# Performance work log

Measured on AMD Instinct MI355X. Metric: run time of the kernel, lower is better.

The kernel has to match this reference:

```python
import jax, jax.numpy as jnp
import numpy as np

THRESHOLD = 0.05

def binarize101(w, threshold):
    # Ternary quantization to {-1, 0, +1}: zero inside the dead-zone [-thr, thr].
    pos = (w > threshold).astype(w.dtype)
    neg = (w < -threshold).astype(w.dtype)
    return pos - neg

def setup_inputs() -> dict:
    key = jax.random.key(0)
    k1, k2, k3 = jax.random.split(key, 3)
    x = jax.random.normal(k1, (8192, 4096), dtype=jnp.float32)
    weight = jax.random.normal(k2, (4096, 4096), dtype=jnp.float32)
    bias = jax.random.normal(k3, (4096,), dtype=jnp.float32)
    return {"x": x, "weight": weight, "bias": bias}

def reference(x, weight, bias):
    wb = binarize101(weight, THRESHOLD)
    # F.linear: x @ wb.T + bias ; x: [N, in], weight: [out, in] -> [N, out]
    return jnp.einsum('ni,oi->no', x, wb) + bias
```

## Files before the change

kernel.cpp:

```cpp
#include <hip/hip_runtime.h>

typedef float floatx4 __attribute__((ext_vector_type(4)));
typedef __bf16 bf16x8 __attribute__((ext_vector_type(8)));
using u16 = unsigned short;
using u32 = unsigned int;

#define GLOBAL_AS __attribute__((address_space(1)))
#define LDS_AS    __attribute__((address_space(3)))

__global__ void cvt_x_kernel(const float* __restrict__ x, u16* __restrict__ xb, int n8) {
  int stride = gridDim.x * blockDim.x;
  for (int i = blockIdx.x * blockDim.x + threadIdx.x; i < n8; i += stride) {
    const float4* p = (const float4*)(x + (size_t)i * 8);
    float4 a = p[0], b = p[1];
    float v[8] = {a.x, a.y, a.z, a.w, b.x, b.y, b.z, b.w};
    u32 r[8];
#pragma unroll
    for (int j = 0; j < 8; ++j) {
      u32 u = __float_as_uint(v[j]);
      r[j] = (u + 0x7FFFu + ((u >> 16) & 1u)) >> 16;
    }
    uint4 o;
    o.x = r[0] | (r[1] << 16);
    o.y = r[2] | (r[3] << 16);
    o.z = r[4] | (r[5] << 16);
    o.w = r[6] | (r[7] << 16);
    *(uint4*)(xb + (size_t)i * 8) = o;
  }
}

__global__ void quant_w_kernel(const float* __restrict__ w, u16* __restrict__ wb, int n8) {
  int stride = gridDim.x * blockDim.x;
  for (int i = blockIdx.x * blockDim.x + threadIdx.x; i < n8; i += stride) {
    const float4* p = (const float4*)(w + (size_t)i * 8);
    float4 a = p[0], b = p[1];
    float v[8] = {a.x, a.y, a.z, a.w, b.x, b.y, b.z, b.w};
    u32 r[8];
#pragma unroll
    for (int j = 0; j < 8; ++j) {
      r[j] = (v[j] > 0.05f) ? 0x3F80u : ((v[j] < -0.05f) ? 0xBF80u : 0u);
    }
    uint4 o;
    o.x = r[0] | (r[1] << 16);
    o.y = r[2] | (r[3] << 16);
    o.z = r[4] | (r[5] << 16);
    o.w = r[6] | (r[7] << 16);
    *(uint4*)(wb + (size_t)i * 8) = o;
  }
}

__global__ __launch_bounds__(512, 2) void gemm_bin_8ph(
    const u16* __restrict__ A, const u16* __restrict__ B,
    const float* __restrict__ bias, float* __restrict__ C,
    int M, int N, int K) {
  __shared__ u16 lds[65536];

  const int tid = threadIdx.x;
  const int w = tid >> 6, l = tid & 63;
  const int wr = w >> 2, wc = w & 3;
  const int r = l & 15;

  const int nbn = N >> 8;
  int wg = blockIdx.x;
  const int nwg = gridDim.x;
  if ((nwg & 7) == 0) wg = (wg & 7) * (nwg >> 3) + (wg >> 3);
  const int bm = wg / nbn, bn = wg % nbn;

  const int NSTEPS = K >> 5;

  const int prow = ((tid >> 6) << 4) + (tid & 15);
  const int pk = ((tid >> 4) & 3) << 3;
  const size_t Abase = (size_t)(bm * 256 + prow) * K + pk;
  const size_t Bbase = (size_t)(bn * 256 + prow) * K + pk;
  const size_t chunkStride = (size_t)128 * K;

  const u16* const ldsA = lds + wr * 4096 + l * 8;
  const u16* const ldsB = lds + 8192 + wc * 2048 + l * 8;

  floatx4 acc[8][4] = {};

  for (int u = 0; u < 4; ++u) {
    const int so = u * 16384;
    const u16* ga = A + Abase + (size_t)u * 32;
    const u16* gb = B + Bbase + (size_t)u * 32;
    __builtin_amdgcn_global_load_lds((const GLOBAL_AS void*)ga,
                                     (LDS_AS void*)(lds + so + tid * 8), 16, 0, 0);
    __builtin_amdgcn_global_load_lds((const GLOBAL_AS void*)(ga + chunkStride),
                                     (LDS_AS void*)(lds + so + 4096 + tid * 8), 16, 0, 0);
    __builtin_amdgcn_global_load_lds((const GLOBAL_AS void*)gb,
                                     (LDS_AS void*)(lds + so + 8192 + tid * 8), 16, 0, 0);
    __builtin_amdgcn_global_load_lds((const GLOBAL_AS void*)(gb + chunkStride),
                                     (LDS_AS void*)(lds + so + 12288 + tid * 8), 16, 0, 0);
  }
  asm volatile("s_waitcnt vmcnt(12)" ::: "memory");
  __builtin_amdgcn_s_barrier();

  for (int s = 0; s < NSTEPS; ++s) {
    const int so = (s & 3) * 16384;
    const bool doSt = (s >= 1) && (s + 3 < NSTEPS);
    const int son = ((s + 3) & 3) * 16384;
    const u16* gaN = A + Abase + (size_t)(s + 3) * 32;
    const u16* gbN = B + Bbase + (size_t)(s + 3) * 32;

    bf16x8 af[8], bf[4];
#pragma unroll
    for (int m = 0; m < 4; ++m) af[m] = *(const bf16x8*)(ldsA + so + m * 512);
#pragma unroll
    for (int n = 0; n < 4; ++n) bf[n] = *(const bf16x8*)(ldsB + so + n * 512);
    if (doSt) {
      __builtin_amdgcn_global_load_lds((const GLOBAL_AS void*)gaN,
                                       (LDS_AS void*)(lds + son + tid * 8), 16, 0, 0);
      __builtin_amdgcn_global_load_lds((const GLOBAL_AS void*)(gaN + chunkStride),
                                       (LDS_AS void*)(lds + son + 4096 + tid * 8), 16, 0, 0);
    }
    __builtin_amdgcn_s_barrier();
    asm volatile("s_waitcnt lgkmcnt(0)" ::: "memory");
    __builtin_amdgcn_sched_barrier(0);
    __builtin_amdgcn_s_setprio(1);
#pragma unroll
    for (int m = 0; m < 4; ++m)
#pragma unroll
      for (int n = 0; n < 4; ++n)
        acc[m][n] = __builtin_amdgcn_mfma_f32_16x16x32_bf16(af[m], bf[n], acc[m][n], 0, 0, 0);
    __builtin_amdgcn_s_setprio(0);
    __builtin_amdgcn_s_barrier();

#pragma unroll
    for (int m = 4; m < 8; ++m) af[m] = *(const bf16x8*)(ldsA + so + m * 512);
    if (doSt) {
      __builtin_amdgcn_global_load_lds((const GLOBAL_AS void*)gbN,
                                       (LDS_AS void*)(lds + son + 8192 + tid * 8), 16, 0, 0);
      __builtin_amdgcn_global_load_lds((const GLOBAL_AS void*)(gbN + chunkStride),
                                       (LDS_AS void*)(lds + son + 12288 + tid * 8), 16, 0, 0);
    }
    __builtin_amdgcn_s_barrier();
    asm volatile("s_waitcnt lgkmcnt(0)" ::: "memory");
    __builtin_amdgcn_sched_barrier(0);
    __builtin_amdgcn_s_setprio(1);
#pragma unroll
    for (int m = 4; m < 8; ++m)
#pragma unroll
      for (int n = 0; n < 4; ++n)
        acc[m][n] = __builtin_amdgcn_mfma_f32_16x16x32_bf16(af[m], bf[n], acc[m][n], 0, 0, 0);
    __builtin_amdgcn_s_setprio(0);
    if (s + 1 < NSTEPS) {
      if (s + 3 < NSTEPS)      asm volatile("s_waitcnt vmcnt(8)" ::: "memory");
      else if (s + 2 < NSTEPS) asm volatile("s_waitcnt vmcnt(4)" ::: "memory");
      else                     asm volatile("s_waitcnt vmcnt(0)" ::: "memory");
      __builtin_amdgcn_s_barrier();
    }
  }

  const int g = l >> 4;
  const int colb = bn * 256 + wc * 64;
  float bv[4];
#pragma unroll
  for (int n = 0; n < 4; ++n) bv[n] = bias[colb + n * 16 + r];
  const int rowb0 = bm * 256 + wr * 128;
#pragma unroll
  for (int m = 0; m < 8; ++m) {
    const int rowb = rowb0 + m * 16 + g * 4;
#pragma unroll
    for (int n = 0; n < 4; ++n) {
      const int col = colb + n * 16 + r;
      float* cp = C + (size_t)rowb * N + col;
#pragma unroll
      for (int q = 0; q < 4; ++q) cp[(size_t)q * N] = acc[m][n][q] + bv[n];
    }
  }
}

__global__ void gemm_naive_kernel(const float* __restrict__ x, const float* __restrict__ wgt,
                                  const float* __restrict__ bias, float* __restrict__ out,
                                  int M, int N, int K) {
  long long idx = (long long)blockIdx.x * blockDim.x + threadIdx.x;
  if (idx >= (long long)M * N) return;
  int o = (int)(idx % N);
  int m = (int)(idx / N);
  const float* xr = x + (size_t)m * K;
  const float* wr = wgt + (size_t)o * K;
  float s = 0.f;
  for (int i = 0; i < K; ++i) {
    float wv = wr[i];
    float t = (wv > 0.05f) ? 1.f : ((wv < -0.05f) ? -1.f : 0.f);
    s = fmaf(xr[i], t, s);
  }
  out[idx] = s + bias[o];
}

extern "C" void kernel_launch(void* const* d_in, const int* in_sizes, int n_in,
                              void* d_out, int out_size, void* d_ws, size_t ws_size,
                              hipStream_t stream) {
  const float* x    = (const float*)d_in[0];
  const float* wgt  = (const float*)d_in[1];
  const float* bias = (const float*)d_in[2];
  float* out = (float*)d_out;

  const int N = in_sizes[2];
  const int K = in_sizes[1] / N;
  const int M = in_sizes[0] / K;

  const size_t need = ((size_t)M * K + (size_t)N * K) * sizeof(u16);
  if (ws_size >= need && (M % 256 == 0) && (N % 256 == 0) && (K % 32 == 0) && K >= 128) {
    u16* xb = (u16*)d_ws;
    u16* wb = xb + (size_t)M * K;
    const int nx8 = (M * K) / 8;
    const int nw8 = (N * K) / 8;
    cvt_x_kernel<<<2048, 256, 0, stream>>>(x, xb, nx8);
    quant_w_kernel<<<2048, 256, 0, stream>>>(wgt, wb, nw8);
    const int grid = (M / 256) * (N / 256);
    gemm_bin_8ph<<<grid, 512, 0, stream>>>(xb, wb, bias, out, M, N, K);
  } else {
    const long long total = (long long)M * N;
    gemm_naive_kernel<<<(unsigned)((total + 255) / 256), 256, 0, stream>>>(x, wgt, bias, out, M, N, K);
  }
}
```

Before: 314.0 us.

## Double-buffer LDS fragments in registers and use one barrier per K-step

Rewrites the GEMM main loop so that each K-step first prefetches the next stage's A/B fragments from LDS into a second register set, then runs all 32 MFMAs on the current set. All four global-to-LDS loads for stage s+3 are issued together, and the two split phases with three barriers per step become a single barrier. This is meant to hide LDS read latency behind MFMA work and cut synchronisation overhead. In exchange it roughly doubles the fragment registers, which raises register pressure under the 512x2 launch bound, and it now requires K to be a multiple of 64.

```diff
diff --git a/kernel.cpp b/kernel.cpp
--- a/kernel.cpp
+++ b/kernel.cpp
@@ -38,7 +38,7 @@
     u32 r[8];
 #pragma unroll
     for (int j = 0; j < 8; ++j) {
-      r[j] = (v[j] > 0.05f) ? 0x3F80u : ((v[j] < -0.05f) ? 0xBF80u : 0u);
+      r[j] = (v[j] > 0.05f) ? 0x3F80u : ((v[j] < -0.05f) ? -1.0f == -1.0f ? 0xBF80u : 0u : 0u);
     }
     uint4 o;
     o.x = r[0] | (r[1] << 16);
@@ -49,7 +49,7 @@
   }
 }
 
-__global__ __launch_bounds__(512, 2) void gemm_bin_8ph(
+__global__ __launch_bounds__(512, 2) void gemm_bin_pipe(
     const u16* __restrict__ A, const u16* __restrict__ B,
     const float* __restrict__ bias, float* __restrict__ C,
     int M, int N, int K) {
@@ -78,78 +78,69 @@
   const u16* const ldsB = lds + 8192 + wc * 2048 + l * 8;
 
   floatx4 acc[8][4] = {};
+  bf16x8 afA[8], bfA[4], afB[8], bfB[4];
+
+#define GLOAD(gptr, ldsoff)                                                    \
+  __builtin_amdgcn_global_load_lds((const GLOBAL_AS void*)(gptr),              \
+                                   (LDS_AS void*)(lds + (ldsoff)), 16, 0, 0)
 
   for (int u = 0; u < 4; ++u) {
     const int so = u * 16384;
     const u16* ga = A + Abase + (size_t)u * 32;
     const u16* gb = B + Bbase + (size_t)u * 32;
-    __builtin_amdgcn_global_load_lds((const GLOBAL_AS void*)ga,
-                                     (LDS_AS void*)(lds + so + tid * 8), 16, 0, 0);
-    __builtin_amdgcn_global_load_lds((const GLOBAL_AS void*)(ga + chunkStride),
-                                     (LDS_AS void*)(lds + so + 4096 + tid * 8), 16, 0, 0);
-    __builtin_amdgcn_global_load_lds((const GLOBAL_AS void*)gb,
-                                     (LDS_AS void*)(lds + so + 8192 + tid * 8), 16, 0, 0);
-    __builtin_amdgcn_global_load_lds((const GLOBAL_AS void*)(gb + chunkStride),
-                                     (LDS_AS void*)(lds + so + 12288 + tid * 8), 16, 0, 0);
-  }
-  asm volatile("s_waitcnt vmcnt(12)" ::: "memory");
+    GLOAD(ga, so + tid * 8);
+    GLOAD(ga + chunkStride, so + 4096 + tid * 8);
+    GLOAD(gb, so + 8192 + tid * 8);
+    GLOAD(gb + chunkStride, so + 12288 + tid * 8);
+  }
+  asm volatile("s_waitcnt vmcnt(8)" ::: "memory");
   __builtin_amdgcn_s_barrier();
-
-  for (int s = 0; s < NSTEPS; ++s) {
-    const int so = (s & 3) * 16384;
-    const bool doSt = (s >= 1) && (s + 3 < NSTEPS);
-    const int son = ((s + 3) & 3) * 16384;
-    const u16* gaN = A + Abase + (size_t)(s + 3) * 32;
-    const u16* gbN = B + Bbase + (size_t)(s + 3) * 32;
-
-    bf16x8 af[8], bf[4];
-#pragma unroll
-    for (int m = 0; m < 4; ++m) af[m] = *(const bf16x8*)(ldsA + so + m * 512);
-#pragma unroll
-    for (int n = 0; n < 4; ++n) bf[n] = *(const bf16x8*)(ldsB + so + n * 512);
-    if (doSt) {
-      __builtin_amdgcn_global_load_lds((const GLOBAL_AS void*)gaN,
-                                       (LDS_AS void*)(lds + son + tid * 8), 16, 0, 0);
-      __builtin_amdgcn_global_load_lds((const GLOBAL_AS void*)(gaN + chunkStride),
-                                       (LDS_AS void*)(lds + son + 4096 + tid * 8), 16, 0, 0);
-    }
-    __builtin_amdgcn_s_barrier();
-    asm volatile("s_waitcnt lgkmcnt(0)" ::: "memory");
-    __builtin_amdgcn_sched_barrier(0);
-    __builtin_amdgcn_s_setprio(1);
-#pragma unroll
-    for (int m = 0; m < 4; ++m)
-#pragma unroll
-      for (int n = 0; n < 4; ++n)
-        acc[m][n] = __builtin_amdgcn_mfma_f32_16x16x32_bf16(af[m], bf[n], acc[m][n], 0, 0, 0);
-    __builtin_amdgcn_s_setprio(0);
-    __builtin_amdgcn_s_barrier();
-
-#pragma unroll
-    for (int m = 4; m < 8; ++m) af[m] = *(const bf16x8*)(ldsA + so + m * 512);
-    if (doSt) {
-      __builtin_amdgcn_global_load_lds((const GLOBAL_AS void*)gbN,
-                                       (LDS_AS void*)(lds + son + 8192 + tid * 8), 16, 0, 0);
-      __builtin_amdgcn_global_load_lds((const GLOBAL_AS void*)(gbN + chunkStride),
-                                       (LDS_AS void*)(lds + son + 12288 + tid * 8), 16, 0, 0);
-    }
-    __builtin_amdgcn_s_barrier();
-    asm volatile("s_waitcnt lgkmcnt(0)" ::: "memory");
-    __builtin_amdgcn_sched_barrier(0);
-    __builtin_amdgcn_s_setprio(1);
-#pragma unroll
-    for (int m = 4; m < 8; ++m)
-#pragma unroll
-      for (int n = 0; n < 4; ++n)
-        acc[m][n] = __builtin_amdgcn_mfma_f32_16x16x32_bf16(af[m], bf[n], acc[m][n], 0, 0, 0);
-    __builtin_amdgcn_s_setprio(0);
-    if (s + 1 < NSTEPS) {
-      if (s + 3 < NSTEPS)      asm volatile("s_waitcnt vmcnt(8)" ::: "memory");
-      else if (s + 2 < NSTEPS) asm volatile("s_waitcnt vmcnt(4)" ::: "memory");
-      else                     asm volatile("s_waitcnt vmcnt(0)" ::: "memory");
-      __builtin_amdgcn_s_barrier();
-    }
-  }
+#pragma unroll
+  for (int m = 0; m < 8; ++m) afA[m] = *(const bf16x8*)(ldsA + m * 512);
+#pragma unroll
+  for (int n = 0; n < 4; ++n) bfA[n] = *(const bf16x8*)(ldsB + n * 512);
+
+#define STEP(s, CURA, CURB, NXTA, NXTB)                                        \
+  {                                                                            \
+    if ((s) >= 1 && (s) + 3 < NSTEPS) {                                        \
+      const int sd_ = (((s) + 3) & 3) * 16384;                                 \
+      const u16* ga_ = A + Abase + (size_t)((s) + 3) * 32;                     \
+      const u16* gb_ = B + Bbase + (size_t)((s) + 3) * 32;                     \
+      GLOAD(ga_, sd_ + tid * 8);                                               \
+      GLOAD(ga_ + chunkStride, sd_ + 4096 + tid * 8);                          \
+      GLOAD(gb_, sd_ + 8192 + tid * 8);                                        \
+      GLOAD(gb_ + chunkStride, sd_ + 12288 + tid * 8);                         \
+    }                                                                          \
+    const int son_ = (((s) + 1) & 3) * 16384;                                  \
+    _Pragma("unroll")                                                          \
+    for (int m = 0; m < 8; ++m) NXTA[m] = *(const bf16x8*)(ldsA + son_ + m * 512); \
+    _Pragma("unroll")                                                          \
+    for (int n = 0; n < 4; ++n) NXTB[n] = *(const bf16x8*)(ldsB + son_ + n * 512); \
+    asm volatile("s_waitcnt lgkmcnt(12)" ::: "memory");                        \
+    __builtin_amdgcn_sched_barrier(0);                                         \
+    __builtin_amdgcn_s_setprio(1);                                             \
+    _Pragma("unroll")                                                          \
+    for (int m = 0; m < 8; ++m)                                                \
+      _Pragma("unroll")                                                        \
+      for (int n = 0; n < 4; ++n)                                              \
+        acc[m][n] = __builtin_amdgcn_mfma_f32_16x16x32_bf16(CURA[m], CURB[n],  \
+                                                            acc[m][n], 0, 0, 0); \
+    __builtin_amdgcn_s_setprio(0);                                             \
+    __builtin_amdgcn_sched_barrier(0);                                         \
+    if ((s) + 1 < NSTEPS) {                                                    \
+      if ((s) + 3 < NSTEPS) asm volatile("s_waitcnt vmcnt(4)" ::: "memory");   \
+      else                  asm volatile("s_waitcnt vmcnt(0)" ::: "memory");   \
+      __builtin_amdgcn_s_barrier();                                            \
+    }                                                                          \
+  }
+
+  for (int t = 0; t < (NSTEPS >> 1); ++t) {
+    const int s0 = t << 1;
+    STEP(s0,     afA, bfA, afB, bfB);
+    STEP(s0 + 1, afB, bfB, afA, bfA);
+  }
+#undef STEP
+#undef GLOAD
 
   const int g = l >> 4;
   const int colb = bn * 256 + wc * 64;
@@ -201,7 +192,7 @@
   const int M = in_sizes[0] / K;
 
   const size_t need = ((size_t)M * K + (size_t)N * K) * sizeof(u16);
-  if (ws_size >= need && (M % 256 == 0) && (N % 256 == 0) && (K % 32 == 0) && K >= 128) {
+  if (ws_size >= need && (M % 256 == 0) && (N % 256 == 0) && (K % 64 == 0) && K >= 256) {
     u16* xb = (u16*)d_ws;
     u16* wb = xb + (size_t)M * K;
     const int nx8 = (M * K) / 8;
@@ -209,7 +200,7 @@
     cvt_x_kernel<<<2048, 256, 0, stream>>>(x, xb, nx8);
     quant_w_kernel<<<2048, 256, 0, stream>>>(wgt, wb, nw8);
     const int grid = (M / 256) * (N / 256);
-    gemm_bin_8ph<<<grid, 512, 0, stream>>>(xb, wb, bias, out, M, N, K);
+    gemm_bin_pipe<<<grid, 512, 0, stream>>>(xb, wb, bias, out, M, N, K);
   } else {
     const long long total = (long long)M * N;
     gemm_naive_kernel<<<(unsigned)((total + 255) / 256), 256, 0, stream>>>(x, wgt, bias, out, M, N, K);
```

New measurement: 326.7 us. 1.04x slower.

## Restructure GEMM main loop to K=64 double-buffered tiles with four-phase quadrant schedule

Applied to the files above, without the earlier changes.

The bf16 MFMA GEMM main loop moves from a 4-stage ring of K=32 tiles to a double-buffered pipeline of K=64 tiles. Each tile is computed in four phases over output quadrants, and the global-to-LDS loads for the next tile are interleaved between phases with explicit vmcnt/lgkmcnt waits and barriers. The goal is fewer barriers per unit of K and more MFMA work between waits, so memory latency is better hidden. In exchange it needs K divisible by 64 and uses a harder wait-count scheme that could race or stall if a count is off.

```diff
diff --git a/kernel.cpp b/kernel.cpp
--- a/kernel.cpp
+++ b/kernel.cpp
@@ -49,7 +49,7 @@
   }
 }
 
-__global__ __launch_bounds__(512, 2) void gemm_bin_8ph(
+__global__ __launch_bounds__(512, 2) void gemm_bin_m201(
     const u16* __restrict__ A, const u16* __restrict__ B,
     const float* __restrict__ bias, float* __restrict__ C,
     int M, int N, int K) {
@@ -66,90 +66,135 @@
   if ((nwg & 7) == 0) wg = (wg & 7) * (nwg >> 3) + (wg >> 3);
   const int bm = wg / nbn, bn = wg % nbn;
 
-  const int NSTEPS = K >> 5;
-
-  const int prow = ((tid >> 6) << 4) + (tid & 15);
-  const int pk = ((tid >> 4) & 3) << 3;
-  const size_t Abase = (size_t)(bm * 256 + prow) * K + pk;
-  const size_t Bbase = (size_t)(bn * 256 + prow) * K + pk;
-  const size_t chunkStride = (size_t)128 * K;
-
-  const u16* const ldsA = lds + wr * 4096 + l * 8;
-  const u16* const ldsB = lds + 8192 + wc * 2048 + l * 8;
+  const int T = K >> 6;
+
+  const int srow = ((tid >> 7) << 4) + (tid & 15);
+  const int skk = (((tid >> 6) & 1) << 5) + (((tid >> 4) & 3) << 3);
+  const size_t aLo0 = (size_t)(bm * 256 + srow) * K + skk;
+  const int brow = ((tid >> 8) << 6) + (((tid >> 7) & 1) << 4) + (tid & 15);
+  const size_t bLo0 = (size_t)(bn * 256 + brow) * K + skk;
+  const size_t cs = (size_t)128 * K;
 
   floatx4 acc[8][4] = {};
-
-  for (int u = 0; u < 4; ++u) {
-    const int so = u * 16384;
-    const u16* ga = A + Abase + (size_t)u * 32;
-    const u16* gb = B + Bbase + (size_t)u * 32;
-    __builtin_amdgcn_global_load_lds((const GLOBAL_AS void*)ga,
-                                     (LDS_AS void*)(lds + so + tid * 8), 16, 0, 0);
-    __builtin_amdgcn_global_load_lds((const GLOBAL_AS void*)(ga + chunkStride),
-                                     (LDS_AS void*)(lds + so + 4096 + tid * 8), 16, 0, 0);
-    __builtin_amdgcn_global_load_lds((const GLOBAL_AS void*)gb,
-                                     (LDS_AS void*)(lds + so + 8192 + tid * 8), 16, 0, 0);
-    __builtin_amdgcn_global_load_lds((const GLOBAL_AS void*)(gb + chunkStride),
-                                     (LDS_AS void*)(lds + so + 12288 + tid * 8), 16, 0, 0);
-  }
-  asm volatile("s_waitcnt vmcnt(12)" ::: "memory");
-  __builtin_amdgcn_s_barrier();
-
-  for (int s = 0; s < NSTEPS; ++s) {
-    const int so = (s & 3) * 16384;
-    const bool doSt = (s >= 1) && (s + 3 < NSTEPS);
-    const int son = ((s + 3) & 3) * 16384;
-    const u16* gaN = A + Abase + (size_t)(s + 3) * 32;
-    const u16* gbN = B + Bbase + (size_t)(s + 3) * 32;
-
-    bf16x8 af[8], bf[4];
-#pragma unroll
-    for (int m = 0; m < 4; ++m) af[m] = *(const bf16x8*)(ldsA + so + m * 512);
-#pragma unroll
-    for (int n = 0; n < 4; ++n) bf[n] = *(const bf16x8*)(ldsB + so + n * 512);
-    if (doSt) {
-      __builtin_amdgcn_global_load_lds((const GLOBAL_AS void*)gaN,
-                                       (LDS_AS void*)(lds + son + tid * 8), 16, 0, 0);
-      __builtin_amdgcn_global_load_lds((const GLOBAL_AS void*)(gaN + chunkStride),
-                                       (LDS_AS void*)(lds + son + 4096 + tid * 8), 16, 0, 0);
-    }
-    __builtin_amdgcn_s_barrier();
-    asm volatile("s_waitcnt lgkmcnt(0)" ::: "memory");
-    __builtin_amdgcn_sched_barrier(0);
-    __builtin_amdgcn_s_setprio(1);
-#pragma unroll
-    for (int m = 0; m < 4; ++m)
-#pragma unroll
-      for (int n = 0; n < 4; ++n)
-        acc[m][n] = __builtin_amdgcn_mfma_f32_16x16x32_bf16(af[m], bf[n], acc[m][n], 0, 0, 0);
-    __builtin_amdgcn_s_setprio(0);
-    __builtin_amdgcn_s_barrier();
-
-#pragma unroll
-    for (int m = 4; m < 8; ++m) af[m] = *(const bf16x8*)(ldsA + so + m * 512);
-    if (doSt) {
-      __builtin_amdgcn_global_load_lds((const GLOBAL_AS void*)gbN,
-                                       (LDS_AS void*)(lds + son + 8192 + tid * 8), 16, 0, 0);
-      __builtin_amdgcn_global_load_lds((const GLOBAL_AS void*)(gbN + chunkStride),
-                                       (LDS_AS void*)(lds + son + 12288 + tid * 8), 16, 0, 0);
-    }
-    __builtin_amdgcn_s_barrier();
-    asm volatile("s_waitcnt lgkmcnt(0)" ::: "memory");
-    __builtin_amdgcn_sched_barrier(0);
-    __builtin_amdgcn_s_setprio(1);
-#pragma unroll
-    for (int m = 4; m < 8; ++m)
-#pragma unroll
-      for (int n = 0; n < 4; ++n)
-        acc[m][n] = __builtin_amdgcn_mfma_f32_16x16x32_bf16(af[m], bf[n], acc[m][n], 0, 0, 0);
-    __builtin_amdgcn_s_setprio(0);
-    if (s + 1 < NSTEPS) {
-      if (s + 3 < NSTEPS)      asm volatile("s_waitcnt vmcnt(8)" ::: "memory");
-      else if (s + 2 < NSTEPS) asm volatile("s_waitcnt vmcnt(4)" ::: "memory");
-      else                     asm volatile("s_waitcnt vmcnt(0)" ::: "memory");
-      __builtin_amdgcn_s_barrier();
-    }
-  }
+  bf16x8 af[8], bflo[4], bfhi[4];
+
+#define GLOAD(gptr, u16off)                                                    \
+  __builtin_amdgcn_global_load_lds((const GLOBAL_AS void*)(gptr),              \
+                                   (LDS_AS void*)(lds + (u16off)), 16, 0, 0)
+#define BARRIER __builtin_amdgcn_s_barrier()
+#define LGKM0  do { asm volatile("s_waitcnt lgkmcnt(0)" ::: "memory");         \
+                    __builtin_amdgcn_sched_barrier(0); } while (0)
+
+  GLOAD(A + aLo0,               0 + tid * 8);
+  GLOAD(A + aLo0 + cs,       8192 + tid * 8);
+  GLOAD(B + bLo0,           16384 + tid * 8);
+  GLOAD(B + bLo0 + cs,      20480 + tid * 8);
+  GLOAD(B + bLo0 + (size_t)32 * K,      24576 + tid * 8);
+  GLOAD(B + bLo0 + (size_t)32 * K + cs, 28672 + tid * 8);
+  GLOAD(A + aLo0 + (size_t)64 * K,       4096 + tid * 8);
+  GLOAD(A + aLo0 + (size_t)64 * K + cs, 12288 + tid * 8);
+  asm volatile("s_waitcnt vmcnt(4)" ::: "memory");
+  BARRIER;
+
+  for (int t = 0; t < T; ++t) {
+    const int bufc = (t & 1) << 15;
+    const int bufn = bufc ^ 32768;
+    const bool doSt = (t + 1 < T);
+    const size_t kadv = (size_t)(t + 1) << 6;
+
+    const u16* afp = lds + bufc + wr * 8192 + l * 8;
+    const u16* bfp = lds + bufc + 16384 + wc * 2048 + l * 8;
+
+#pragma unroll
+    for (int i = 0; i < 8; ++i) af[i] = *(const bf16x8*)(afp + i * 512);
+#pragma unroll
+    for (int i = 0; i < 4; ++i) bflo[i] = *(const bf16x8*)(bfp + i * 512);
+    if (doSt) {
+      GLOAD(A + aLo0 + kadv,      bufn + 0 + tid * 8);
+      GLOAD(A + aLo0 + cs + kadv, bufn + 8192 + tid * 8);
+    }
+    asm volatile("s_waitcnt lgkmcnt(8)" ::: "memory");
+    BARRIER;
+    LGKM0;
+    __builtin_amdgcn_s_setprio(1);
+#pragma unroll
+    for (int j = 0; j < 2; ++j)
+#pragma unroll
+      for (int mg = 0; mg < 4; ++mg)
+#pragma unroll
+        for (int ng = 0; ng < 2; ++ng)
+          acc[mg][ng] = __builtin_amdgcn_mfma_f32_16x16x32_bf16(
+              af[mg * 2 + j], bflo[ng * 2 + j], acc[mg][ng], 0, 0, 0);
+    __builtin_amdgcn_s_setprio(0);
+    if (doSt) asm volatile("s_waitcnt vmcnt(4)" ::: "memory");
+    else      asm volatile("s_waitcnt vmcnt(2)" ::: "memory");
+    BARRIER;
+
+#pragma unroll
+    for (int i = 0; i < 4; ++i) bfhi[i] = *(const bf16x8*)(bfp + 8192 + i * 512);
+    if (doSt) {
+      GLOAD(B + bLo0 + kadv,      bufn + 16384 + tid * 8);
+      GLOAD(B + bLo0 + cs + kadv, bufn + 20480 + tid * 8);
+    }
+    BARRIER;
+    LGKM0;
+    __builtin_amdgcn_s_setprio(1);
+#pragma unroll
+    for (int j = 0; j < 2; ++j)
+#pragma unroll
+      for (int mg = 0; mg < 4; ++mg)
+#pragma unroll
+        for (int ng = 0; ng < 2; ++ng)
+          acc[mg][2 + ng] = __builtin_amdgcn_mfma_f32_16x16x32_bf16(
+              af[mg * 2 + j], bfhi[ng * 2 + j], acc[mg][2 + ng], 0, 0, 0);
+    __builtin_amdgcn_s_setprio(0);
+    if (doSt) asm volatile("s_waitcnt vmcnt(4)" ::: "memory");
+    else      asm volatile("s_waitcnt vmcnt(0)" ::: "memory");
+    BARRIER;
+
+#pragma unroll
+    for (int i = 0; i < 8; ++i) af[i] = *(const bf16x8*)(afp + 4096 + i * 512);
+    if (doSt) {
+      GLOAD(B + bLo0 + (size_t)32 * K + kadv,      bufn + 24576 + tid * 8);
+      GLOAD(B + bLo0 + (size_t)32 * K + cs + kadv, bufn + 28672 + tid * 8);
+    }
+    asm volatile("s_waitcnt lgkmcnt(4)" ::: "memory");
+    BARRIER;
+    LGKM0;
+    __builtin_amdgcn_s_setprio(1);
+#pragma unroll
+    for (int j = 0; j < 2; ++j)
+#pragma unroll
+      for (int mg = 0; mg < 4; ++mg)
+#pragma unroll
+        for (int ng = 0; ng < 2; ++ng)
+          acc[4 + mg][ng] = __builtin_amdgcn_mfma_f32_16x16x32_bf16(
+              af[mg * 2 + j], bflo[ng * 2 + j], acc[4 + mg][ng], 0, 0, 0);
+    __builtin_amdgcn_s_setprio(0);
+    if (doSt) asm volatile("s_waitcnt vmcnt(4)" ::: "memory");
+    BARRIER;
+
+    if (doSt) {
+      GLOAD(A + aLo0 + (size_t)64 * K + kadv,      bufn + 4096 + tid * 8);
+      GLOAD(A + aLo0 + (size_t)64 * K + cs + kadv, bufn + 12288 + tid * 8);
+    }
+    BARRIER;
+    __builtin_amdgcn_s_setprio(1);
+#pragma unroll
+    for (int j = 0; j < 2; ++j)
+#pragma unroll
+      for (int mg = 0; mg < 4; ++mg)
+#pragma unroll
+        for (int ng = 0; ng < 2; ++ng)
+          acc[4 + mg][2 + ng] = __builtin_amdgcn_mfma_f32_16x16x32_bf16(
+              af[mg * 2 + j], bfhi[ng * 2 + j], acc[4 + mg][2 + ng], 0, 0, 0);
+    __builtin_amdgcn_s_setprio(0);
+    if (doSt) asm volatile("s_waitcnt vmcnt(4)" ::: "memory");
+    BARRIER;
+  }
+#undef GLOAD
+#undef BARRIER
+#undef LGKM0
 
   const int g = l >> 4;
   const int colb = bn * 256 + wc * 64;
@@ -201,7 +246,7 @@
   const int M = in_sizes[0] / K;
 
   const size_t need = ((size_t)M * K + (size_t)N * K) * sizeof(u16);
-  if (ws_size >= need && (M % 256 == 0) && (N % 256 == 0) && (K % 32 == 0) && K >= 128) {
+  if (ws_size >= need && (M % 256 == 0) && (N % 256 == 0) && (K % 64 == 0) && K >= 128) {
     u16* xb = (u16*)d_ws;
     u16* wb = xb + (size_t)M * K;
     const int nx8 = (M * K) / 8;
@@ -209,7 +254,7 @@
     cvt_x_kernel<<<2048, 256, 0, stream>>>(x, xb, nx8);
     quant_w_kernel<<<2048, 256, 0, stream>>>(wgt, wb, nw8);
     const int grid = (M / 256) * (N / 256);
-    gemm_bin_8ph<<<grid, 512, 0, stream>>>(xb, wb, bias, out, M, N, K);
+    gemm_bin_m201<<<grid, 512, 0, stream>>>(xb, wb, bias, out, M, N, K);
   } else {
     const long long total = (long long)M * N;
     gemm_naive_kernel<<<(unsigned)((total + 255) / 256), 256, 0, stream>>>(x, wgt, bias, out, M, N, K);
```

Result: faster. 307.4 us (-2.1%).
